# Kernel optimization log

Hardware: AMD Instinct MI355X
Metric: run time of the kernel (lower is better)

Reference implementation:

```python
import jax, jax.numpy as jnp
import numpy as np

B, M, C, D, FF, FEAT = 1, 1024, 128, 512, 1024, 20
PAIR = 3 * D + 2 * FEAT  # slow_scorer_size = 1576


def _ffnn(x, W0, b0, W1, b1):
    # FFNN(depth=1): hidden relu layer then linear output (eval mode, no dropout)
    return jax.nn.relu(x @ W0 + b0) @ W1 + b1


def _batch_gather(x, idx):
    # x: [B, M, ...], idx: [B, ...] int -> gather along mention dim per batch
    return jax.vmap(lambda xb, ib: xb[ib])(x, idx)


def _bucket_distance(d):
    # log-scale distance buckets 0..9 (identity for d<=4)
    log_idx = jnp.floor(jnp.log(jnp.maximum(d, 1).astype(jnp.float32)) / jnp.log(2.0)).astype(jnp.int32) + 3
    return jnp.clip(jnp.where(d <= 4, d, log_idx), 0, 9)


def setup_inputs() -> dict:
    key = jax.random.key(0)
    ks = jax.random.split(key, 10)
    s = 0.02
    return {
        'mention_emb': jax.random.normal(ks[0], (B, M, D), dtype=jnp.float32),
        'mention_cluster_ids': jax.random.randint(ks[1], (B, M), 0, 200),
        'mention_speaker_ids': jax.random.randint(ks[2], (B, M), 0, 2),
        'ms_W0': jax.random.normal(ks[3], (D, FF), dtype=jnp.float32) * s,
        'ms_b0': jnp.zeros((FF,), jnp.float32),
        'ms_W1': jax.random.normal(ks[4], (FF, 1), dtype=jnp.float32) * s,
        'ms_b1': jnp.zeros((1,), jnp.float32),
        'sp_W0': jax.random.normal(ks[5], (PAIR, FF), dtype=jnp.float32) * s,
        'sp_b0': jnp.zeros((FF,), jnp.float32),
        'sp_W1': jax.random.normal(ks[6], (FF, 1), dtype=jnp.float32) * s,
        'sp_b1': jnp.zeros((1,), jnp.float32),
        'speaker_emb': jax.random.normal(ks[7], (2, FEAT), dtype=jnp.float32) * s,
        'bucket_emb': jax.random.normal(ks[8], (10, FEAT), dtype=jnp.float32) * s,
    }


def reference(mention_emb, mention_cluster_ids, mention_speaker_ids,
              ms_W0, ms_b0, ms_W1, ms_b1,
              sp_W0, sp_b0, sp_W1, sp_b1,
              speaker_emb, bucket_emb):
    # mention scoring
    mention_scores = _ffnn(mention_emb, ms_W0, ms_b0, ms_W1, ms_b1)[..., 0]  # [B, M]

    # get_antecedent_info: fixed window of C previous mentions
    offsets = jnp.arange(1, C + 1)[None, None, :]                    # [1,1,C]
    raw = jnp.arange(M)[None, :, None] - offsets                      # [1,M,C]
    antecedents = jnp.broadcast_to(jnp.clip(raw, 0, M - 1), (B, M, C))
    ant_mask = jnp.broadcast_to(raw >= 0, (B, M, C))

    fast_scores = _batch_gather(mention_scores, antecedents) + mention_scores[:, :, None]
    antecedent_emb = _batch_gather(mention_emb, antecedents)          # [B,M,C,D]

    # slow pair scorer features
    same_speaker = (_batch_gather(mention_speaker_ids, antecedents) == mention_speaker_ids[:, :, None]).astype(jnp.int32)
    speaker_feat = speaker_emb[same_speaker]                          # [B,M,C,FEAT]
    bucket_feat = jnp.broadcast_to(bucket_emb[_bucket_distance(offsets)], (B, M, C, FEAT))

    src = jnp.broadcast_to(mention_emb[:, :, None, :], (B, M, C, D))
    pair_emb = jnp.concatenate([src, antecedent_emb, src * antecedent_emb, speaker_feat, bucket_feat], axis=-1)
    slow_scores = _ffnn(pair_emb, sp_W0, sp_b0, sp_W1, sp_b1)[..., 0]  # [B,M,C]

    antecedent_scores = fast_scores + slow_scores + jnp.log(ant_mask.astype(jnp.float32))
    overall_scores = jnp.concatenate([jnp.zeros((B, M, 1), jnp.float32), antecedent_scores], axis=2)
    overall_dist = jax.nn.softmax(overall_scores, axis=-1)
    eps = 1e-6
    overall_dist = jnp.clip(overall_dist, eps, 1.0 - eps)
    overall_dist = overall_dist / jnp.sum(overall_dist, axis=-1, keepdims=True)

    # coref loss from cluster ids
    ant_cluster = _batch_gather(mention_cluster_ids, antecedents) * ant_mask.astype(mention_cluster_ids.dtype)
    same_cluster = ant_cluster == mention_cluster_ids[:, :, None]
    non_dummy = (mention_cluster_ids > 0)[:, :, None]
    ant_labels = same_cluster & non_dummy
    dummy_labels = ~jnp.any(ant_labels, axis=2, keepdims=True)
    overall_labels = jnp.concatenate([dummy_labels, ant_labels], axis=2)
    loss = -jnp.sum(jnp.log(overall_dist) * overall_labels.astype(jnp.float32), axis=2)
    loss = jnp.mean(jnp.sum(loss, axis=1))
    return overall_dist, loss
```

## Files before the change

kernel.cpp:

```cpp
#include <hip/hip_runtime.h>
#include <math.h>

#define MM 1024
#define DD 512
#define CC 128
#define LDSR 516


typedef __attribute__((ext_vector_type(8))) short bf16x8;
typedef __attribute__((ext_vector_type(4), aligned(8))) short bf16x4a;
typedef __attribute__((ext_vector_type(4))) float f32x4;

__device__ __forceinline__ ushort bf16_rn(float x) {
    uint u = __float_as_uint(x);
    uint r = u + 0x7fffu + ((u >> 16) & 1u);
    return (ushort)(r >> 16);
}
__device__ __forceinline__ float bf16_to_f(ushort u) {
    return __uint_as_float(((uint)u) << 16);
}
__device__ __forceinline__ bf16x8 ld_lds16(const ushort* p) {
    bf16x4a lo = *(const bf16x4a*)p;
    bf16x4a hi = *(const bf16x4a*)(p + 4);
    return __builtin_shufflevector(lo, hi, 0, 1, 2, 3, 4, 5, 6, 7);
}

__global__ __launch_bounds__(256) void prep_emb(const float* __restrict__ emb,
                                                ushort* __restrict__ embb)
{
    int i = blockIdx.x * 256 + threadIdx.x;
    float2 v = ((const float2*)emb)[i];
    ushort2 o;
    o.x = bf16_rn(v.x);
    o.y = bf16_rn(v.y);
    ((ushort2*)embb)[i] = o;
}

__global__ __launch_bounds__(256) void prep_wall(const float* __restrict__ ms_W0,
                                                 const float* __restrict__ sp_W0,
                                                 ushort* __restrict__ Wall)
{
    __shared__ float t[64][65];
    const int k0 = blockIdx.x * 64;
    const int n0 = blockIdx.y * 64;
    const int g = n0 >> 10;
    const float* src = (g == 0) ? ms_W0 : (sp_W0 + (size_t)(g - 1) * 512 * 1024);
    const int col0 = n0 & 1023;
    const int tr = threadIdx.x >> 6, tc = threadIdx.x & 63;
#pragma unroll
    for (int i = 0; i < 16; ++i) {
        int k = tr + i * 4;
        t[k][tc] = src[(size_t)(k0 + k) * 1024 + col0 + tc];
    }
    __syncthreads();
    const int f = threadIdx.x >> 2;
    const int c4 = threadIdx.x & 3;
    ushort tmp[16];
#pragma unroll
    for (int j = 0; j < 16; ++j) tmp[j] = bf16_rn(t[c4 * 16 + j][f]);
    uint4* dst = (uint4*)(Wall + (size_t)(n0 + f) * 512 + k0 + c4 * 16);
    dst[0] = *(uint4*)&tmp[0];
    dst[1] = *(uint4*)&tmp[8];
}

__global__ __launch_bounds__(64) void prep_wfrag16(const float* __restrict__ W,
                                                   ushort* __restrict__ dst_frag)
{
    const int ts = blockIdx.x;
    const int l = threadIdx.x;
    const int t16 = ts >> 4, s = ts & 15;
    const int f = t16 * 16 + (l & 15);
    const int kb = s * 32 + ((l >> 4) & 3) * 8;
    ushort tmp[8];
#pragma unroll
    for (int j = 0; j < 8; ++j) tmp[j] = bf16_rn(W[(size_t)(kb + j) * 1024 + f]);
    uint4* dst = (uint4*)(dst_frag + ((size_t)ts * 64 + l) * 8);
    *dst = *(uint4*)&tmp[0];
}

__global__ __launch_bounds__(256) void gemm_h_mfma(
    const ushort* __restrict__ embb, const ushort* __restrict__ Wall,
    float* __restrict__ H)
{
    const int n0 = blockIdx.x * 128;
    const int m0 = blockIdx.y * 128;
    const int lane = threadIdx.x & 63, wave = threadIdx.x >> 6;
    const int wx = wave & 1, wy = wave >> 1;
    const int l15 = lane & 15, lq = lane >> 4;

    const ushort* arow[4];
#pragma unroll
    for (int mi = 0; mi < 4; ++mi)
        arow[mi] = embb + (size_t)(m0 + wy * 64 + mi * 16 + l15) * 512;
    const ushort* brow[4];
#pragma unroll
    for (int ni = 0; ni < 4; ++ni)
        brow[ni] = Wall + (size_t)(n0 + wx * 64 + ni * 16 + l15) * 512;

    f32x4 acc[4][4];
#pragma unroll
    for (int i = 0; i < 4; ++i)
#pragma unroll
        for (int j = 0; j < 4; ++j) acc[i][j] = (f32x4)0.f;

    for (int kt = 0; kt < 512; kt += 32) {
        const int ko = kt + lq * 8;
        bf16x8 av[4], bv[4];
#pragma unroll
        for (int mi = 0; mi < 4; ++mi) av[mi] = *(const bf16x8*)(arow[mi] + ko);
#pragma unroll
        for (int ni = 0; ni < 4; ++ni) bv[ni] = *(const bf16x8*)(brow[ni] + ko);
#pragma unroll
        for (int mi = 0; mi < 4; ++mi)
#pragma unroll
            for (int ni = 0; ni < 4; ++ni)
                acc[mi][ni] = __builtin_amdgcn_mfma_f32_16x16x32_bf16(av[mi], bv[ni], acc[mi][ni], 0, 0, 0);
    }
#pragma unroll
    for (int mi = 0; mi < 4; ++mi)
#pragma unroll
        for (int r = 0; r < 4; ++r) {
            int mrow = m0 + wy * 64 + mi * 16 + lq * 4 + r;
#pragma unroll
            for (int ni = 0; ni < 4; ++ni)
                H[(size_t)mrow * 3072 + n0 + wx * 64 + ni * 16 + l15] = acc[mi][ni][r];
        }
}

__global__ void small_proj(const float* __restrict__ speaker_emb,
                           const float* __restrict__ bucket_emb,
                           const float* __restrict__ sp_W0,
                           float* __restrict__ spk_proj, float* __restrict__ bkt_proj)
{
    int r = blockIdx.x;
    const float* e; const float* W; float* out;
    if (r < 2) { e = speaker_emb + r * 20; W = sp_W0 + (size_t)1536 * 1024; out = spk_proj + r * 1024; }
    else       { e = bucket_emb + (r - 2) * 20; W = sp_W0 + (size_t)1556 * 1024; out = bkt_proj + (r - 2) * 1024; }
    float ek[20];
#pragma unroll
    for (int k = 0; k < 20; ++k) ek[k] = e[k];
    for (int f = threadIdx.x; f < 1024; f += blockDim.x) {
        float s = 0.f;
#pragma unroll
        for (int k = 0; k < 20; ++k) s = fmaf(ek[k], W[(size_t)k * 1024 + f], s);
        out[f] = s;
    }
}

__global__ __launch_bounds__(256) void mention_score(
    const float* __restrict__ H, const float* __restrict__ ms_b0,
    const float* __restrict__ ms_W1, const float* __restrict__ ms_b1,
    float* __restrict__ ms)
{
    int m = blockIdx.x;
    float v = 0.f;
    for (int f = threadIdx.x; f < 1024; f += 256) {
        float h = H[(size_t)m * 3072 + f] + ms_b0[f];
        v += fmaxf(h, 0.f) * ms_W1[f];
    }
#pragma unroll
    for (int o = 1; o < 64; o <<= 1) v += __shfl_xor(v, o);
    __shared__ float sm[4];
    if ((threadIdx.x & 63) == 0) sm[threadIdx.x >> 6] = v;
    __syncthreads();
    if (threadIdx.x == 0) ms[m] = sm[0] + sm[1] + sm[2] + sm[3] + ms_b1[0];
}

__global__ __launch_bounds__(512, 8) void pair_mfma(
    const ushort* __restrict__ embb, const ushort* __restrict__ Wfrag16,
    const float* __restrict__ H, const float* __restrict__ spk_proj,
    const float* __restrict__ bkt_proj, const float* __restrict__ sp_b0,
    const float* __restrict__ sp_W1, const int* __restrict__ speaker,
    float* __restrict__ slow0, float* __restrict__ slow1)
{
    extern __shared__ ushort Alds[];
    float* red = (float*)(Alds + 32 * LDSR);
    int* meta_ss = (int*)(red + 8 * 32);
    int* meta_bk = meta_ss + 32;
    const int m = blockIdx.x;
    const int cq = blockIdx.y & 3;
    const int fh = blockIdx.y >> 2;
    const int cbase = cq * 32;
    const int tid = threadIdx.x;
    const int spk_m = speaker[m];

    {
        const int c = tid & 31;
        const int kh = (tid >> 5) * 32;
        int a = m - 1 - (cbase + c); if (a < 0) a = 0;
        const ushort* ea = embb + (size_t)a * 512 + kh;
        const ushort* em = embb + (size_t)m * 512 + kh;
        ushort* dst = Alds + c * LDSR + kh;
#pragma unroll
        for (int j = 0; j < 32; j += 8) {
            bf16x8 va = *(const bf16x8*)(ea + j);
            bf16x8 vm = *(const bf16x8*)(em + j);
            uint pr[4];
#pragma unroll
            for (int p = 0; p < 4; ++p) {
                float q0 = bf16_to_f((ushort)va[2 * p])     * bf16_to_f((ushort)vm[2 * p]);
                float q1 = bf16_to_f((ushort)va[2 * p + 1]) * bf16_to_f((ushort)vm[2 * p + 1]);
                pr[p] = __builtin_amdgcn_perm(__float_as_uint(q1), __float_as_uint(q0), 0x07060302u);
            }
            *(uint2*)(dst + j)     = *(uint2*)&pr[0];
            *(uint2*)(dst + j + 4) = *(uint2*)&pr[2];
        }
        if (tid < 32) {
            meta_ss[c] = (speaker[a] == spk_m) ? 1 : 0;
            int off = cbase + c + 1;
            int bk;
            if (off <= 4) bk = off;
            else { bk = 31 - __clz(off) + 3; if (bk > 9) bk = 9; }
            meta_bk[c] = bk;
        }
    }
    __syncthreads();

    const int lane = tid & 63;
    const int wave = __builtin_amdgcn_readfirstlane(tid >> 6);
    const int l15 = lane & 15, lq = lane >> 4;
    const ushort* ab0 = Alds + l15 * LDSR + lq * 8;

#pragma unroll 1
    for (int ft2 = 0; ft2 < 2; ++ft2) {
        const int f0a = fh * 512 + wave * 64 + ft2 * 32;
        const ushort* bb0 = Wfrag16 + (size_t)(fh * 32 + wave * 4 + ft2 * 2) * 8192
                                    + (size_t)lane * 8;
        f32x4 acc[2][2];
#pragma unroll
        for (int i = 0; i < 2; ++i)
#pragma unroll
            for (int j = 0; j < 2; ++j) acc[i][j] = (f32x4)0.f;

#pragma unroll 2
        for (int s = 0; s < 16; ++s) {
            bf16x8 b0 = *(const bf16x8*)(bb0 + s * 512);
            bf16x8 b1 = *(const bf16x8*)(bb0 + 8192 + s * 512);
            bf16x8 a0 = ld_lds16(ab0 + s * 32);
            bf16x8 a1 = ld_lds16(ab0 + 16 * LDSR + s * 32);
            __builtin_amdgcn_s_setprio(1);
            acc[0][0] = __builtin_amdgcn_mfma_f32_16x16x32_bf16(a0, b0, acc[0][0], 0, 0, 0);
            acc[0][1] = __builtin_amdgcn_mfma_f32_16x16x32_bf16(a0, b1, acc[0][1], 0, 0, 0);
            acc[1][0] = __builtin_amdgcn_mfma_f32_16x16x32_bf16(a1, b0, acc[1][0], 0, 0, 0);
            acc[1][1] = __builtin_amdgcn_mfma_f32_16x16x32_bf16(a1, b1, acc[1][1], 0, 0, 0);
            __builtin_amdgcn_s_setprio(0);
        }

        float srcb[2], w1v[2], sp0v[2], sp1v[2];
#pragma unroll
        for (int fi = 0; fi < 2; ++fi) {
            int fcol = f0a + fi * 16 + l15;
            srcb[fi] = H[(size_t)m * 3072 + 1024 + fcol] + sp_b0[fcol];
            w1v[fi]  = sp_W1[fcol];
            sp0v[fi] = spk_proj[fcol];
            sp1v[fi] = spk_proj[1024 + fcol];
        }
#pragma unroll
        for (int ct = 0; ct < 2; ++ct) {
#pragma unroll
            for (int reg = 0; reg < 4; ++reg) {
                const int cl = ct * 16 + lq * 4 + reg;
                int a = m - 1 - (cbase + cl); if (a < 0) a = 0;
                const int ss = meta_ss[cl];
                const int bk = meta_bk[cl];
                const float* antp = H + (size_t)a * 3072 + 2048;
                float s = 0.f;
#pragma unroll
                for (int fi = 0; fi < 2; ++fi) {
                    const int fcol = f0a + fi * 16 + l15;
                    float bval = bkt_proj[(size_t)bk * 1024 + fcol];
                    float pre = acc[ct][fi][reg] + srcb[fi] + antp[fcol]
                              + (ss ? sp1v[fi] : sp0v[fi]) + bval;
                    s += fmaxf(pre, 0.f) * w1v[fi];
                }
                s += __shfl_xor(s, 1); s += __shfl_xor(s, 2);
                s += __shfl_xor(s, 4); s += __shfl_xor(s, 8);
                if (l15 == 0) {
                    if (ft2 == 0) red[wave * 32 + cl] = s;
                    else          red[wave * 32 + cl] += s;
                }
            }
        }
    }
    __syncthreads();
    if (tid < 32) {
        float s = 0.f;
#pragma unroll
        for (int i = 0; i < 8; ++i) s += red[i * 32 + tid];
        float* sout = fh ? slow1 : slow0;
        sout[(size_t)m * 128 + cbase + tid] = s;
    }
}

__device__ __forceinline__ float bsum2(float v, float* sm) {
#pragma unroll
    for (int o = 1; o < 64; o <<= 1) v += __shfl_xor(v, o);
    __syncthreads();
    if ((threadIdx.x & 63) == 0) sm[threadIdx.x >> 6] = v;
    __syncthreads();
    return sm[0] + sm[1];
}
__device__ __forceinline__ float bmax2(float v, float* sm) {
#pragma unroll
    for (int o = 1; o < 64; o <<= 1) v = fmaxf(v, __shfl_xor(v, o));
    __syncthreads();
    if ((threadIdx.x & 63) == 0) sm[threadIdx.x >> 6] = v;
    __syncthreads();
    return fmaxf(sm[0], sm[1]);
}

__global__ __launch_bounds__(128) void softmax_loss(
    const float* __restrict__ slow0, const float* __restrict__ slow1,
    const float* __restrict__ ms,
    const float* __restrict__ sp_b1, const int* __restrict__ cluster,
    float* __restrict__ out, float* __restrict__ loss_partial)
{
    const int m = blockIdx.x, c = threadIdx.x;
    __shared__ float sm[2];
    const int raw = m - 1 - c;
    const bool maskv = raw >= 0;
    const int a = maskv ? raw : 0;
    float score = slow0[(size_t)m * 128 + c] + slow1[(size_t)m * 128 + c]
                + sp_b1[0] + ms[m] + ms[a];
    if (!maskv) score = -INFINITY;

    float mx = fmaxf(bmax2(score, sm), 0.f);
    float e = expf(score - mx);
    float e0 = expf(0.f - mx);
    float sum = bsum2(e, sm) + e0;
    float p = e / sum, p0 = e0 / sum;
    const float eps = 1e-6f;
    p  = fminf(fmaxf(p,  eps), 1.f - eps);
    p0 = fminf(fmaxf(p0, eps), 1.f - eps);
    float sum2 = bsum2(p, sm) + p0;
    p /= sum2; p0 /= sum2;
    out[(size_t)m * 129 + 1 + c] = p;
    if (c == 0) out[(size_t)m * 129] = p0;

    const int cid = cluster[m];
    const bool lbl = maskv && (cid > 0) && (cluster[a] == cid);
    float anyc = bsum2(lbl ? 1.f : 0.f, sm);
    float lsum = bsum2(lbl ? -logf(p) : 0.f, sm);
    if (c == 0) {
        if (anyc == 0.f) lsum += -logf(p0);
        loss_partial[m] = lsum;
    }
}

__global__ void loss_sum(const float* __restrict__ lp, float* __restrict__ out) {
    float v = 0.f;
    for (int i = threadIdx.x; i < 1024; i += 256) v += lp[i];
#pragma unroll
    for (int o = 1; o < 64; o <<= 1) v += __shfl_xor(v, o);
    __shared__ float sm[4];
    if ((threadIdx.x & 63) == 0) sm[threadIdx.x >> 6] = v;
    __syncthreads();
    if (threadIdx.x == 0) out[(size_t)1024 * 129] = sm[0] + sm[1] + sm[2] + sm[3];
}

extern "C" void kernel_launch(void* const* d_in, const int* in_sizes, int n_in,
                              void* d_out, int out_size, void* d_ws, size_t ws_size,
                              hipStream_t stream)
{
    const float* emb   = (const float*)d_in[0];
    const int*   clus  = (const int*)  d_in[1];
    const int*   spk   = (const int*)  d_in[2];
    const float* ms_W0 = (const float*)d_in[3];
    const float* ms_b0 = (const float*)d_in[4];
    const float* ms_W1 = (const float*)d_in[5];
    const float* ms_b1 = (const float*)d_in[6];
    const float* sp_W0 = (const float*)d_in[7];
    const float* sp_b0 = (const float*)d_in[8];
    const float* sp_W1 = (const float*)d_in[9];
    const float* sp_b1 = (const float*)d_in[10];
    const float* spke  = (const float*)d_in[11];
    const float* bkte  = (const float*)d_in[12];

    float* ws = (float*)d_ws;
    float* H        = ws;
    float* slow0    = ws + 3145728;
    float* spk_proj = ws + 3276800;
    float* bkt_proj = ws + 3278848;
    float* msc      = ws + 3289088;
    float* lossp    = ws + 3290112;
    ushort* embb    = (ushort*)(ws + 3291136);
    ushort* Wall    = (ushort*)(ws + 3553280);
    ushort* Wfrag16 = Wall + (size_t)3072 * 512;
    float* slow1    = ws + 4601856;
    float* out = (float*)d_out;

    const int pair_lds = 32 * LDSR * 2 + 8 * 32 * 4 + 2 * 32 * 4;

    static bool attr_set = false;
    if (!attr_set) {
        hipFuncSetAttribute((const void*)&pair_mfma,
                            hipFuncAttributeMaxDynamicSharedMemorySize,
                            pair_lds);
        attr_set = true;
    }

    hipLaunchKernelGGL(prep_emb, dim3(1024), dim3(256), 0, stream, emb, embb);
    hipLaunchKernelGGL(prep_wall, dim3(8, 48), dim3(256), 0, stream, ms_W0, sp_W0, Wall);
    hipLaunchKernelGGL(prep_wfrag16, dim3(1024), dim3(64), 0, stream,
                       sp_W0 + (size_t)1024 * 1024, Wfrag16);
    hipLaunchKernelGGL(gemm_h_mfma, dim3(24, 8), dim3(256), 0, stream, embb, Wall, H);
    hipLaunchKernelGGL(small_proj, dim3(12), dim3(256), 0, stream, spke, bkte, sp_W0, spk_proj, bkt_proj);
    hipLaunchKernelGGL(mention_score, dim3(1024), dim3(256), 0, stream, H, ms_b0, ms_W1, ms_b1, msc);
    hipLaunchKernelGGL(pair_mfma, dim3(1024, 8), dim3(512), pair_lds, stream,
                       embb, Wfrag16, H, spk_proj, bkt_proj, sp_b0, sp_W1, spk, slow0, slow1);
    hipLaunchKernelGGL(softmax_loss, dim3(1024), dim3(128), 0, stream,
                       slow0, slow1, msc, sp_b1, clus, out, lossp);
    hipLaunchKernelGGL(loss_sum, dim3(1), dim3(256), 0, stream, lossp, out);
}
```

Before: 360.8 us.

## Cover all 1024 features per pair block, halving grid and A-tile staging

The pair kernel previously split the feature dimension across two blocks (fh), each staging the same src*antecedent A tile in LDS and writing separate partial outputs slow0/slow1. Now each block loops over four 32-feature tiles covering all 1024 features, accumulates partial scores in registers, and does a single shuffle reduction at the end. The weight fragments are re-laid out so each wave's B loads for a k-step are contiguous. This removes duplicate LDS staging and the extra output buffer and read in softmax, but doubles the per-block serial work and halves the number of blocks.

Result: faster. 347.9 us (-3.6%).

```diff
diff --git a/kernel.cpp b/kernel.cpp
--- a/kernel.cpp
+++ b/kernel.cpp
@@ -63,18 +63,20 @@
     dst[1] = *(uint4*)&tmp[8];
 }
 
-__global__ __launch_bounds__(64) void prep_wfrag16(const float* __restrict__ W,
-                                                   ushort* __restrict__ dst_frag)
-{
-    const int ts = blockIdx.x;
+__global__ __launch_bounds__(64) void prep_wfragP(const float* __restrict__ W,
+                                                  ushort* __restrict__ dst_frag)
+{
+    const int bid = blockIdx.x;
     const int l = threadIdx.x;
-    const int t16 = ts >> 4, s = ts & 15;
+    const int g2 = bid >> 5, s = (bid >> 1) & 15, j = bid & 1;
+    const int wave = g2 >> 2, ft = g2 & 3;
+    const int t16 = wave * 8 + ft * 2 + j;
     const int f = t16 * 16 + (l & 15);
     const int kb = s * 32 + ((l >> 4) & 3) * 8;
     ushort tmp[8];
 #pragma unroll
-    for (int j = 0; j < 8; ++j) tmp[j] = bf16_rn(W[(size_t)(kb + j) * 1024 + f]);
-    uint4* dst = (uint4*)(dst_frag + ((size_t)ts * 64 + l) * 8);
+    for (int e = 0; e < 8; ++e) tmp[e] = bf16_rn(W[(size_t)(kb + e) * 1024 + f]);
+    uint4* dst = (uint4*)(dst_frag + (size_t)bid * 512 + l * 8);
     *dst = *(uint4*)&tmp[0];
 }
 
@@ -167,19 +169,18 @@
 }
 
 __global__ __launch_bounds__(512, 8) void pair_mfma(
-    const ushort* __restrict__ embb, const ushort* __restrict__ Wfrag16,
+    const ushort* __restrict__ embb, const ushort* __restrict__ WfragP,
     const float* __restrict__ H, const float* __restrict__ spk_proj,
     const float* __restrict__ bkt_proj, const float* __restrict__ sp_b0,
     const float* __restrict__ sp_W1, const int* __restrict__ speaker,
-    float* __restrict__ slow0, float* __restrict__ slow1)
+    float* __restrict__ slow)
 {
     extern __shared__ ushort Alds[];
     float* red = (float*)(Alds + 32 * LDSR);
     int* meta_ss = (int*)(red + 8 * 32);
     int* meta_bk = meta_ss + 32;
     const int m = blockIdx.x;
-    const int cq = blockIdx.y & 3;
-    const int fh = blockIdx.y >> 2;
+    const int cq = blockIdx.y;
     const int cbase = cq * 32;
     const int tid = threadIdx.x;
     const int spk_m = speaker[m];
@@ -221,21 +222,29 @@
     const int l15 = lane & 15, lq = lane >> 4;
     const ushort* ab0 = Alds + l15 * LDSR + lq * 8;
 
+    const float* Hsrc = H + m * 3072 + 1024;
+    const float* Hant = H + 2048;
+
+    float sacc[2][4];
+#pragma unroll
+    for (int ct = 0; ct < 2; ++ct)
+#pragma unroll
+        for (int r = 0; r < 4; ++r) sacc[ct][r] = 0.f;
+
 #pragma unroll 1
-    for (int ft2 = 0; ft2 < 2; ++ft2) {
-        const int f0a = fh * 512 + wave * 64 + ft2 * 32;
-        const ushort* bb0 = Wfrag16 + (size_t)(fh * 32 + wave * 4 + ft2 * 2) * 8192
-                                    + (size_t)lane * 8;
+    for (int ft = 0; ft < 4; ++ft) {
+        const int f0a = wave * 128 + ft * 32;
+        const ushort* bb = WfragP + (size_t)(wave * 4 + ft) * 16384 + (size_t)lane * 8;
         f32x4 acc[2][2];
 #pragma unroll
         for (int i = 0; i < 2; ++i)
 #pragma unroll
             for (int j = 0; j < 2; ++j) acc[i][j] = (f32x4)0.f;
 
-#pragma unroll 2
+#pragma unroll 4
         for (int s = 0; s < 16; ++s) {
-            bf16x8 b0 = *(const bf16x8*)(bb0 + s * 512);
-            bf16x8 b1 = *(const bf16x8*)(bb0 + 8192 + s * 512);
+            bf16x8 b0 = *(const bf16x8*)(bb + s * 1024);
+            bf16x8 b1 = *(const bf16x8*)(bb + s * 1024 + 512);
             bf16x8 a0 = ld_lds16(ab0 + s * 32);
             bf16x8 a1 = ld_lds16(ab0 + 16 * LDSR + s * 32);
             __builtin_amdgcn_s_setprio(1);
@@ -249,8 +258,8 @@
         float srcb[2], w1v[2], sp0v[2], sp1v[2];
 #pragma unroll
         for (int fi = 0; fi < 2; ++fi) {
-            int fcol = f0a + fi * 16 + l15;
-            srcb[fi] = H[(size_t)m * 3072 + 1024 + fcol] + sp_b0[fcol];
+            const int fcol = f0a + fi * 16 + l15;
+            srcb[fi] = Hsrc[fcol] + sp_b0[fcol];
             w1v[fi]  = sp_W1[fcol];
             sp0v[fi] = spk_proj[fcol];
             sp1v[fi] = spk_proj[1024 + fcol];
@@ -262,24 +271,30 @@
                 const int cl = ct * 16 + lq * 4 + reg;
                 int a = m - 1 - (cbase + cl); if (a < 0) a = 0;
                 const int ss = meta_ss[cl];
-                const int bk = meta_bk[cl];
-                const float* antp = H + (size_t)a * 3072 + 2048;
-                float s = 0.f;
+                const int aidx = a * 3072;
+                const int bidx = meta_bk[cl] << 10;
+                float s = sacc[ct][reg];
 #pragma unroll
                 for (int fi = 0; fi < 2; ++fi) {
                     const int fcol = f0a + fi * 16 + l15;
-                    float bval = bkt_proj[(size_t)bk * 1024 + fcol];
-                    float pre = acc[ct][fi][reg] + srcb[fi] + antp[fcol]
+                    float bval = bkt_proj[bidx + fcol];
+                    float pre = acc[ct][fi][reg] + srcb[fi] + Hant[aidx + fcol]
                               + (ss ? sp1v[fi] : sp0v[fi]) + bval;
                     s += fmaxf(pre, 0.f) * w1v[fi];
                 }
-                s += __shfl_xor(s, 1); s += __shfl_xor(s, 2);
-                s += __shfl_xor(s, 4); s += __shfl_xor(s, 8);
-                if (l15 == 0) {
-                    if (ft2 == 0) red[wave * 32 + cl] = s;
-                    else          red[wave * 32 + cl] += s;
-                }
+                sacc[ct][reg] = s;
             }
+        }
+    }
+
+#pragma unroll
+    for (int ct = 0; ct < 2; ++ct) {
+#pragma unroll
+        for (int reg = 0; reg < 4; ++reg) {
+            float s = sacc[ct][reg];
+            s += __shfl_xor(s, 1); s += __shfl_xor(s, 2);
+            s += __shfl_xor(s, 4); s += __shfl_xor(s, 8);
+            if (l15 == 0) red[wave * 32 + ct * 16 + lq * 4 + reg] = s;
         }
     }
     __syncthreads();
@@ -287,8 +302,7 @@
         float s = 0.f;
 #pragma unroll
         for (int i = 0; i < 8; ++i) s += red[i * 32 + tid];
-        float* sout = fh ? slow1 : slow0;
-        sout[(size_t)m * 128 + cbase + tid] = s;
+        slow[m * 128 + cbase + tid] = s;
     }
 }
 
@@ -310,8 +324,7 @@
 }
 
 __global__ __launch_bounds__(128) void softmax_loss(
-    const float* __restrict__ slow0, const float* __restrict__ slow1,
-    const float* __restrict__ ms,
+    const float* __restrict__ slow, const float* __restrict__ ms,
     const float* __restrict__ sp_b1, const int* __restrict__ cluster,
     float* __restrict__ out, float* __restrict__ loss_partial)
 {
@@ -320,8 +333,7 @@
     const int raw = m - 1 - c;
     const bool maskv = raw >= 0;
     const int a = maskv ? raw : 0;
-    float score = slow0[(size_t)m * 128 + c] + slow1[(size_t)m * 128 + c]
-                + sp_b1[0] + ms[m] + ms[a];
+    float score = slow[(size_t)m * 128 + c] + sp_b1[0] + ms[m] + ms[a];
     if (!maskv) score = -INFINITY;
 
     float mx = fmaxf(bmax2(score, sm), 0.f);
@@ -378,15 +390,14 @@
 
     float* ws = (float*)d_ws;
     float* H        = ws;
-    float* slow0    = ws + 3145728;
+    float* slow     = ws + 3145728;
     float* spk_proj = ws + 3276800;
     float* bkt_proj = ws + 3278848;
     float* msc      = ws + 3289088;
     float* lossp    = ws + 3290112;
     ushort* embb    = (ushort*)(ws + 3291136);
     ushort* Wall    = (ushort*)(ws + 3553280);
-    ushort* Wfrag16 = Wall + (size_t)3072 * 512;
-    float* slow1    = ws + 4601856;
+    ushort* WfragP  = Wall + (size_t)3072 * 512;
     float* out = (float*)d_out;
 
     const int pair_lds = 32 * LDSR * 2 + 8 * 32 * 4 + 2 * 32 * 4;
@@ -401,14 +412,14 @@
 
     hipLaunchKernelGGL(prep_emb, dim3(1024), dim3(256), 0, stream, emb, embb);
     hipLaunchKernelGGL(prep_wall, dim3(8, 48), dim3(256), 0, stream, ms_W0, sp_W0, Wall);
-    hipLaunchKernelGGL(prep_wfrag16, dim3(1024), dim3(64), 0, stream,
-                       sp_W0 + (size_t)1024 * 1024, Wfrag16);
+    hipLaunchKernelGGL(prep_wfragP, dim3(1024), dim3(64), 0, stream,
+                       sp_W0 + (size_t)1024 * 1024, WfragP);
     hipLaunchKernelGGL(gemm_h_mfma, dim3(24, 8), dim3(256), 0, stream, embb, Wall, H);
     hipLaunchKernelGGL(small_proj, dim3(12), dim3(256), 0, stream, spke, bkte, sp_W0, spk_proj, bkt_proj);
     hipLaunchKernelGGL(mention_score, dim3(1024), dim3(256), 0, stream, H, ms_b0, ms_W1, ms_b1, msc);
-    hipLaunchKernelGGL(pair_mfma, dim3(1024, 8), dim3(512), pair_lds, stream,
-                       embb, Wfrag16, H, spk_proj, bkt_proj, sp_b0, sp_W1, spk, slow0, slow1);
+    hipLaunchKernelGGL(pair_mfma, dim3(1024, 4), dim3(512), pair_lds, stream,
+                       embb, WfragP, H, spk_proj, bkt_proj, sp_b0, sp_W1, spk, slow);
     hipLaunchKernelGGL(softmax_loss, dim3(1024), dim3(128), 0, stream,
-                       slow0, slow1, msc, sp_b1, clus, out, lossp);
+                       slow, msc, sp_b1, clus, out, lossp);
     hipLaunchKernelGGL(loss_sum, dim3(1), dim3(256), 0, stream, lossp, out);
 }
```
